# Performance work log

Hardware: AMD Instinct MI355X
Metric: run time of the kernel (lower is better)

Reference implementation:

```python
import jax, jax.numpy as jnp
import numpy as np

D_MODEL = 1024
N_EXPERTS = 8
HIDDEN = ((int(round(D_MODEL * (8.0 / 3.0))) + 63) // 64) * 64  # 2752
ALPHA = 0.05  # load_balance_alpha


def setup_inputs() -> dict:
    key = jax.random.key(0)
    ks = jax.random.split(key, 6)
    s = 0.02
    x = jax.random.normal(ks[0], (4, 1024, D_MODEL), dtype=jnp.float32)
    Wg = jax.random.normal(ks[1], (D_MODEL, N_EXPERTS), dtype=jnp.float32) * s
    bg = jnp.zeros((N_EXPERTS,), dtype=jnp.float32)
    Wu = jax.random.normal(ks[2], (N_EXPERTS, D_MODEL, HIDDEN), dtype=jnp.float32) * s
    Wv = jax.random.normal(ks[3], (N_EXPERTS, D_MODEL, HIDDEN), dtype=jnp.float32) * s
    Wd = jax.random.normal(ks[4], (N_EXPERTS, HIDDEN, D_MODEL), dtype=jnp.float32) * s
    return {"x": x, "Wg": Wg, "bg": bg, "Wu": Wu, "Wv": Wv, "Wd": Wd}


def reference(x, Wg, bg, Wu, Wv, Wd):
    b, t, d = x.shape
    E = Wu.shape[0]
    xf = x.reshape(b * t, d)  # [N, d]

    # Top-1 router
    logits = xf @ Wg + bg                      # [N, E]
    probs = jax.nn.softmax(logits, axis=-1)
    top1_idx = jnp.argmax(probs, axis=-1)      # [N]
    top1_p = jnp.max(probs, axis=-1)           # [N]
    onehot = jax.nn.one_hot(top1_idx, E, dtype=x.dtype)  # [N, E]

    # Load-balancing aux loss (both me and ce are under no_grad in the original)
    me = jax.lax.stop_gradient(onehot.mean(axis=0))
    ce = jax.lax.stop_gradient(probs.mean(axis=0))
    aux = ALPHA * E * jnp.sum(me * ce)

    # Dropless dispatch: masked per-expert SwiGLU (loop over small fixed E)
    gate = onehot * top1_p[:, None]            # [N, E] combine weights
    y = jnp.zeros_like(xf)
    for e in range(E):
        u = xf @ Wu[e]                         # [N, H]
        v = xf @ Wv[e]                         # [N, H]
        ye = (jax.nn.silu(u) * v) @ Wd[e]      # [N, d]
        y = y + gate[:, e, None] * ye

    return y.reshape(b, t, d), aux
```

## Files before the change

kernel.cpp:

```cpp
#include <hip/hip_runtime.h>

#define D_MODEL 1024
#define HID     2752
#define NEXP    8
#define NTOK    4096
#define ALPHA   0.05f

#define TILES_UV  (43 * 16 * 16)
#define TILES_WD  (16 * 43 * 8)
#define RTR_BLKS  1024

#define TS 66

typedef __bf16 bf16_t;
typedef bf16_t bf16x8 __attribute__((ext_vector_type(8)));
typedef float  f32x4  __attribute__((ext_vector_type(4)));
typedef float  vf4    __attribute__((ext_vector_type(4)));

__device__ inline unsigned short f2bf(float f) {
    unsigned int u = __float_as_uint(f);
    u += 0x7fffu + ((u >> 16) & 1u);
    return (unsigned short)(u >> 16);
}

__device__ inline bf16x8 ldsFrag(const unsigned short* p) {
    union { uint4 u; bf16x8 b; } t;
    t.u = *(const uint4*)p;
    return t.b;
}

__device__ inline void gload_lds16(const void* g, void* l) {
    __builtin_amdgcn_global_load_lds((const __attribute__((address_space(1))) void*)g,
                                     (__attribute__((address_space(3))) void*)l, 16, 0, 0);
}

__global__ __launch_bounds__(256) void prep_kernel(
    const float* __restrict__ x, const float* __restrict__ Wg, const float* __restrict__ bg,
    const float* __restrict__ Wu, const float* __restrict__ Wv, const float* __restrict__ Wd,
    unsigned short* __restrict__ WuT, unsigned short* __restrict__ WvT,
    unsigned short* __restrict__ WdT,
    int* __restrict__ eidx, float* __restrict__ gate_p,
    int* __restrict__ counts, float* __restrict__ ce_sum,
    unsigned short* __restrict__ xbf, int nTiles) {

    __shared__ __align__(16) unsigned short tile[64 * TS];
    const int id = blockIdx.x;
    const int tid = threadIdx.x;

    if (id < nTiles) {
        const int z  = id / 688;
        const int rm = id - z * 688;
        const int bx = rm % 43;
        const int by = rm / 43;
        const float* src;
        unsigned short* dst;
        int R, C, r0, c0;
        if (z < 16) {
            const int e = z & 7;
            src = ((z < 8) ? Wu : Wv) + (size_t)e * D_MODEL * HID;
            dst = ((z < 8) ? WuT : WvT) + (size_t)e * D_MODEL * HID;
            R = D_MODEL; C = HID;
            r0 = by * 64; c0 = bx * 64;
        } else {
            const int e = z - 16;
            src = Wd + (size_t)e * HID * D_MODEL;
            dst = WdT + (size_t)e * HID * D_MODEL;
            R = HID; C = D_MODEL;
            r0 = bx * 64; c0 = by * 64;
        }
#pragma unroll
        for (int j = 0; j < 4; ++j) {
            int f = j * 256 + tid;
            int row = f >> 4, c4 = (f & 15) * 4;
            vf4 v = __builtin_nontemporal_load(
                (const vf4*)(src + (size_t)(r0 + row) * C + c0 + c4));
            unsigned int p0 = (unsigned)f2bf(v.x) | ((unsigned)f2bf(v.y) << 16);
            unsigned int p1 = (unsigned)f2bf(v.z) | ((unsigned)f2bf(v.w) << 16);
            unsigned int* tp = (unsigned int*)&tile[row * TS + c4];
            tp[0] = p0; tp[1] = p1;
        }
        __syncthreads();
#pragma unroll
        for (int j = 0; j < 2; ++j) {
            int f = j * 256 + tid;
            int oc = f >> 3, kc = f & 7;
            unsigned int w[4];
#pragma unroll
            for (int q = 0; q < 4; ++q) {
                unsigned int lo = tile[(kc * 8 + 2 * q)     * TS + oc];
                unsigned int hi = tile[(kc * 8 + 2 * q + 1) * TS + oc];
                w[q] = lo | (hi << 16);
            }
            uint4 out; out.x = w[0]; out.y = w[1]; out.z = w[2]; out.w = w[3];
            *(uint4*)(dst + (size_t)(c0 + oc) * R + r0 + kc * 8) = out;
        }
        return;
    }

    float* ceS = (float*)tile;
    int*   cntS = (int*)tile + 8;
    if (tid < 8) { ceS[tid] = 0.f; cntS[tid] = 0; }
    __syncthreads();

    const int rid = id - nTiles;
    const int wid = tid >> 6, lane = tid & 63;
    const int t = rid * 4 + wid;
    const float* xr = x + (size_t)t * D_MODEL;
    unsigned short* xbr = xbf + (size_t)t * D_MODEL;

    float acc[8];
#pragma unroll
    for (int e = 0; e < 8; ++e) acc[e] = 0.f;

#pragma unroll
    for (int c = 0; c < 4; ++c) {
        int i0 = c * 256 + lane * 4;
        float4 xv = *(const float4*)(xr + i0);
        uint2 pk;
        pk.x = (unsigned)f2bf(xv.x) | ((unsigned)f2bf(xv.y) << 16);
        pk.y = (unsigned)f2bf(xv.z) | ((unsigned)f2bf(xv.w) << 16);
        *(uint2*)(xbr + i0) = pk;
#pragma unroll
        for (int j = 0; j < 4; ++j) {
            const float* wr = Wg + (size_t)(i0 + j) * 8;
            float4 lo = *(const float4*)(wr);
            float4 hi = *(const float4*)(wr + 4);
            float xs = (&xv.x)[j];
            acc[0] += xs * lo.x; acc[1] += xs * lo.y;
            acc[2] += xs * lo.z; acc[3] += xs * lo.w;
            acc[4] += xs * hi.x; acc[5] += xs * hi.y;
            acc[6] += xs * hi.z; acc[7] += xs * hi.w;
        }
    }
#pragma unroll
    for (int e = 0; e < 8; ++e) {
#pragma unroll
        for (int off = 32; off > 0; off >>= 1)
            acc[e] += __shfl_xor(acc[e], off, 64);
    }

    if (lane == 0) {
        float lg[8];
#pragma unroll
        for (int e = 0; e < 8; ++e) lg[e] = acc[e] + bg[e];
        float mx = lg[0]; int am = 0;
#pragma unroll
        for (int e = 1; e < 8; ++e) { if (lg[e] > mx) { mx = lg[e]; am = e; } }
        float ex[8], s = 0.f;
#pragma unroll
        for (int e = 0; e < 8; ++e) { ex[e] = __expf(lg[e] - mx); s += ex[e]; }
        float inv = 1.f / s;
#pragma unroll
        for (int e = 0; e < 8; ++e) atomicAdd(&ceS[e], ex[e] * inv);
        atomicAdd(&cntS[am], 1);
        eidx[t] = am;
        gate_p[t] = ex[am] * inv;
    }
    __syncthreads();
    if (tid < 8) atomicAdd(&ce_sum[tid], ceS[tid]);
    if (tid >= 8 && tid < 16) atomicAdd(&counts[tid - 8], cntS[tid - 8]);
}

__global__ __launch_bounds__(256) void transpose_kernel(const float* __restrict__ in,
                                                        unsigned short* __restrict__ out,
                                                        int R, int C) {
    __shared__ float tile[64 * 65];
    const int e = blockIdx.z;
    const float* src = in + (size_t)e * R * C;
    unsigned short* dst = out + (size_t)e * R * C;
    const int c0 = blockIdx.x * 64, r0 = blockIdx.y * 64;
    const int tid = threadIdx.x;
#pragma unroll
    for (int j = 0; j < 4; ++j) {
        int f = j * 256 + tid;
        int row = f >> 4, c4 = f & 15;
        float4 v = *(const float4*)(src + (size_t)(r0 + row) * C + c0 + c4 * 4);
        float* t = &tile[row * 65 + c4 * 4];
        t[0] = v.x; t[1] = v.y; t[2] = v.z; t[3] = v.w;
    }
    __syncthreads();
#pragma unroll
    for (int j = 0; j < 2; ++j) {
        int f = j * 256 + tid;
        int orow = f >> 3, kc = f & 7;
        unsigned short pk[8];
#pragma unroll
        for (int q = 0; q < 8; ++q) pk[q] = f2bf(tile[(kc * 8 + q) * 65 + orow]);
        *(uint4*)(dst + (size_t)(c0 + orow) * R + r0 + kc * 8) = *(uint4*)pk;
    }
}

__global__ void offsets_aux_kernel(const int* __restrict__ counts, const float* __restrict__ ce_sum,
                                   int* __restrict__ offs, float* __restrict__ aux_out) {
    if (threadIdx.x == 0) {
        int off = 0; float aux = 0.f;
        for (int e = 0; e < 8; ++e) {
            offs[e] = off; off += counts[e];
            aux += ((float)counts[e] / (float)NTOK) * (ce_sum[e] / (float)NTOK);
        }
        aux_out[0] = ALPHA * (float)NEXP * aux;
    }
}

__global__ void scatter_kernel(const int* __restrict__ eidx, const int* __restrict__ offs,
                               int* __restrict__ fill, int* __restrict__ toks) {
    int t = blockIdx.x * 256 + threadIdx.x;
    int e = eidx[t];
    int pos = atomicAdd(&fill[e], 1);
    toks[offs[e] + pos] = t;
}

__global__ __launch_bounds__(256, 2) void gemm1_kernel(
    const unsigned short* __restrict__ WuT, const unsigned short* __restrict__ WvT,
    const unsigned short* __restrict__ xbf,
    const int* __restrict__ toks, const int* __restrict__ counts, const int* __restrict__ offs,
    unsigned short* __restrict__ hbuf) {
    const int e = blockIdx.z;
    const int Ne = counts[e];
    const int mt = blockIdx.y;
    if (mt * 128 >= Ne) return;
    const int nt = blockIdx.x;
    const int slot0 = offs[e] + mt * 128;
    const int rowsV = min(128, Ne - mt * 128);
    const int ncol0 = nt * 128;
    const int colsV = min(128, HID - ncol0);

    __shared__ unsigned short As[128 * 64];
    __shared__ unsigned short Bus[128 * 64];
    __shared__ unsigned short Bvs[128 * 64];

    const int tid = threadIdx.x;

    const unsigned short* aS[4];
    const unsigned short* buS[4];
    const unsigned short* bvS[4];
    unsigned short* aD[4];
    unsigned short* buD[4];
    unsigned short* bvD[4];
#pragma unroll
    for (int i = 0; i < 4; ++i) {
        int c = i * 256 + tid;
        int r = c >> 3, ch = c & 7;
        int srcOff = ((ch ^ (r & 7)) * 8);
        int ar = min(r, rowsV - 1);
        int tok = toks[slot0 + ar];
        aS[i] = xbf + (size_t)tok * D_MODEL + srcOff;
        int bn = ncol0 + min(r, colsV - 1);
        buS[i] = WuT + ((size_t)e * HID + bn) * D_MODEL + srcOff;
        bvS[i] = WvT + ((size_t)e * HID + bn) * D_MODEL + srcOff;
        aD[i]  = As  + c * 8;
        buD[i] = Bus + c * 8;
        bvD[i] = Bvs + c * 8;
    }

    f32x4 accU[4][4], accV[4][4];
#pragma unroll
    for (int m = 0; m < 4; ++m)
#pragma unroll
        for (int n = 0; n < 4; ++n) {
            accU[m][n] = (f32x4){0.f, 0.f, 0.f, 0.f};
            accV[m][n] = (f32x4){0.f, 0.f, 0.f, 0.f};
        }

    const int lane = tid & 63;
    const int w = tid >> 6;
    const int rbase = (w >> 1) * 64;
    const int cbase = (w & 1) * 64;
    const int lrow = lane & 15;
    const int lchunk = lane >> 4;

    for (int ks = 0; ks < 16; ++ks) {
#pragma unroll
        for (int i = 0; i < 4; ++i) gload_lds16(aS[i],  aD[i]);
#pragma unroll
        for (int i = 0; i < 4; ++i) gload_lds16(buS[i], buD[i]);
#pragma unroll
        for (int i = 0; i < 4; ++i) gload_lds16(bvS[i], bvD[i]);
#pragma unroll
        for (int i = 0; i < 4; ++i) { aS[i] += 64; buS[i] += 64; bvS[i] += 64; }
        __syncthreads();

#pragma unroll
        for (int kk = 0; kk < 2; ++kk) {
            const int g = kk * 4 + lchunk;
            bf16x8 af[4], bu[4], bv[4];
#pragma unroll
            for (int m = 0; m < 4; ++m) {
                int r = rbase + m * 16 + lrow;
                af[m] = ldsFrag(&As[r * 64 + ((g ^ (r & 7)) * 8)]);
            }
#pragma unroll
            for (int n = 0; n < 4; ++n) {
                int rn = cbase + n * 16 + lrow;
                int off = rn * 64 + ((g ^ (rn & 7)) * 8);
                bu[n] = ldsFrag(&Bus[off]);
                bv[n] = ldsFrag(&Bvs[off]);
            }
#pragma unroll
            for (int m = 0; m < 4; ++m)
#pragma unroll
                for (int n = 0; n < 4; ++n) {
                    accU[m][n] = __builtin_amdgcn_mfma_f32_16x16x32_bf16(af[m], bu[n], accU[m][n], 0, 0, 0);
                    accV[m][n] = __builtin_amdgcn_mfma_f32_16x16x32_bf16(af[m], bv[n], accV[m][n], 0, 0, 0);
                }
        }
        __syncthreads();
    }

#pragma unroll
    for (int m = 0; m < 4; ++m) {
#pragma unroll
        for (int i = 0; i < 4; ++i) {
            int r = rbase + m * 16 + (lane >> 4) * 4 + i;
            if (r >= rowsV) continue;
            size_t rowOff = (size_t)(slot0 + r) * HID + ncol0;
#pragma unroll
            for (int n = 0; n < 4; ++n) {
                int c = cbase + n * 16 + (lane & 15);
                if (c < colsV) {
                    float u = accU[m][n][i];
                    float v = accV[m][n][i];
                    float s = u / (1.f + __expf(-u));
                    hbuf[rowOff + c] = f2bf(s * v);
                }
            }
        }
    }
}


#define G2_STAGE(AS, BS)                                                  \
    {                                                                     \
        _Pragma("unroll")                                                 \
        for (int i = 0; i < 4; ++i) { gload_lds16(aS[i], &AS[aOff[i]]); aS[i] += 64; } \
        _Pragma("unroll")                                                 \
        for (int i = 0; i < 2; ++i) { gload_lds16(bS[i], &BS[bOff[i]]); bS[i] += 64; } \
    }

#define G2_COMPUTE(AS, BS)                                                \
    {                                                                     \
        _Pragma("unroll")                                                 \
        for (int kk = 0; kk < 2; ++kk) {                                  \
            const int g = kk * 4 + lchunk;                                \
            bf16x8 af[4], bf[2];                                          \
            _Pragma("unroll")                                             \
            for (int m = 0; m < 4; ++m) {                                 \
                int r = rbase + m * 16 + lrow;                            \
                af[m] = ldsFrag(&AS[r * 64 + ((g ^ (r & 7)) * 8)]);       \
            }                                                             \
            _Pragma("unroll")                                             \
            for (int n = 0; n < 2; ++n) {                                 \
                int rn = cbase + n * 16 + lrow;                           \
                bf[n] = ldsFrag(&BS[rn * 64 + ((g ^ (rn & 7)) * 8)]);     \
            }                                                             \
            __builtin_amdgcn_s_setprio(1);                                \
            _Pragma("unroll")                                             \
            for (int m = 0; m < 4; ++m)                                   \
                _Pragma("unroll")                                         \
                for (int n = 0; n < 2; ++n)                               \
                    acc[m][n] = __builtin_amdgcn_mfma_f32_16x16x32_bf16(af[m], bf[n], acc[m][n], 0, 0, 0); \
            __builtin_amdgcn_s_setprio(0);                                \
        }                                                                 \
    }

__global__ __launch_bounds__(256, 2) void gemm2_kernel(
    const unsigned short* __restrict__ WdT, const unsigned short* __restrict__ hbuf,
    const int* __restrict__ toks, const int* __restrict__ counts, const int* __restrict__ offs,
    const float* __restrict__ gate_p, float* __restrict__ yout) {
    const int id = blockIdx.x;
    const int e  = id & 7;
    const int j  = id >> 3;
    const int mt = j & 31;
    const int nt = j >> 5;
    const int Ne = counts[e];
    if (mt * 128 >= Ne) return;
    const int slot0 = offs[e] + mt * 128;
    const int rowsV = min(128, Ne - mt * 128);
    const int ncol0 = nt * 64;

    __shared__ unsigned short As0[128 * 64];
    __shared__ unsigned short As1[128 * 64];
    __shared__ unsigned short Bs0[64 * 64];
    __shared__ unsigned short Bs1[64 * 64];

    const int tid = threadIdx.x;

    const unsigned short* aS[4];
    int aOff[4];
#pragma unroll
    for (int i = 0; i < 4; ++i) {
        int c = i * 256 + tid;
        int r = c >> 3, ch = c & 7;
        int srcOff = (ch ^ (r & 7)) * 8;
        int ar = min(r, rowsV - 1);
        aS[i] = hbuf + (size_t)(slot0 + ar) * HID + srcOff;
        aOff[i] = c * 8;
    }
    const unsigned short* bS[2];
    int bOff[2];
#pragma unroll
    for (int i = 0; i < 2; ++i) {
        int c = i * 256 + tid;
        int r = c >> 3, ch = c & 7;
        int srcOff = (ch ^ (r & 7)) * 8;
        bS[i] = WdT + ((size_t)e * D_MODEL + ncol0 + r) * HID + srcOff;
        bOff[i] = c * 8;
    }

    f32x4 acc[4][2];
#pragma unroll
    for (int m = 0; m < 4; ++m)
#pragma unroll
        for (int n = 0; n < 2; ++n) acc[m][n] = (f32x4){0.f, 0.f, 0.f, 0.f};

    const int lane = tid & 63;
    const int w = tid >> 6;
    const int rbase = (w >> 1) * 64;
    const int cbase = (w & 1) * 32;
    const int lrow = lane & 15;
    const int lchunk = lane >> 4;

    G2_STAGE(As0, Bs0);
    __syncthreads();

#pragma unroll 1
    for (int k2 = 0; k2 < 21; ++k2) {
        G2_STAGE(As1, Bs1);
        G2_COMPUTE(As0, Bs0);
        __syncthreads();
        G2_STAGE(As0, Bs0);
        G2_COMPUTE(As1, Bs1);
        __syncthreads();
    }
    G2_COMPUTE(As0, Bs0);

#pragma unroll
    for (int m = 0; m < 4; ++m) {
#pragma unroll
        for (int i = 0; i < 4; ++i) {
            int r = rbase + m * 16 + (lane >> 4) * 4 + i;
            if (r >= rowsV) continue;
            int tok = toks[slot0 + r];
            float p = gate_p[tok];
            float* yrow = yout + (size_t)tok * D_MODEL + ncol0;
#pragma unroll
            for (int n = 0; n < 2; ++n) {
                int c = cbase + n * 16 + (lane & 15);
                yrow[c] = p * acc[m][n][i];
            }
        }
    }
}

extern "C" void kernel_launch(void* const* d_in, const int* in_sizes, int n_in,
                              void* d_out, int out_size, void* d_ws, size_t ws_size,
                              hipStream_t stream) {
    const float* x  = (const float*)d_in[0];
    const float* Wg = (const float*)d_in[1];
    const float* bg = (const float*)d_in[2];
    const float* Wu = (const float*)d_in[3];
    const float* Wv = (const float*)d_in[4];
    const float* Wd = (const float*)d_in[5];
    float* yout = (float*)d_out;
    float* aux_out = yout + (size_t)NTOK * D_MODEL;

    char* ws = (char*)d_ws;
    int*   counts = (int*)(ws + 0);
    int*   offs   = (int*)(ws + 32);
    float* ce_sum = (float*)(ws + 64);
    int*   fill   = (int*)(ws + 96);
    int*   eidx   = (int*)(ws + 128);
    float* gate_p = (float*)(ws + 16512);
    int*   toks   = (int*)(ws + 32896);
    unsigned short* xbf  = (unsigned short*)(ws + 65536);
    unsigned short* hbuf = (unsigned short*)(ws + 8454144);
    unsigned short* WuT  = (unsigned short*)(ws + 30998528);
    unsigned short* WvT  = (unsigned short*)(ws + 76087296);
    const size_t WDT_OFF = 121176064;
    const size_t WDT_SZ  = (size_t)NEXP * D_MODEL * HID * 2;
    const bool sepWdT = ws_size >= WDT_OFF + WDT_SZ;
    unsigned short* WdT = sepWdT ? (unsigned short*)(ws + WDT_OFF) : WuT;

    const int nTiles = sepWdT ? (TILES_UV + TILES_WD) : TILES_UV;

    (void)hipMemsetAsync(ws, 0, 128, stream);
    prep_kernel<<<nTiles + RTR_BLKS, 256, 0, stream>>>(
        x, Wg, bg, Wu, Wv, Wd, WuT, WvT, WdT,
        eidx, gate_p, counts, ce_sum, xbf, nTiles);
    offsets_aux_kernel<<<1, 64, 0, stream>>>(counts, ce_sum, offs, aux_out);
    scatter_kernel<<<16, 256, 0, stream>>>(eidx, offs, fill, toks);
    gemm1_kernel<<<dim3(22, 32, 8), 256, 0, stream>>>(WuT, WvT, xbf, toks, counts, offs, hbuf);
    if (!sepWdT)
        transpose_kernel<<<dim3(D_MODEL / 64, HID / 64, 8), 256, 0, stream>>>(Wd, WdT, HID, D_MODEL);
    gemm2_kernel<<<8 * 32 * 16, 256, 0, stream>>>(WdT, hbuf, toks, counts, offs, gate_p, yout);
}
```

Before: 252.0 us.

## Double-buffer gemm1 with 128x64 tiles, fine-grained waitcnt sync, fuse offsets into scatter

Gemm1 switches from 128x128 single-buffered tiles to 128x64 tiles with double-buffered LDS. Global-to-LDS loads for the next k-step now overlap MFMA compute, using explicit vmcnt waits, raw barriers and sched barriers. MFMA issue runs at raised priority. Gemm2 swaps __syncthreads for the same partial vmcnt waits. The offsets/aux kernel is folded into the scatter kernel, which removes one launch. The smaller N tile doubles A (x) reloads and the grid size, and the hand-written waitcnt counts are fragile if the number of loads changes.

```diff
diff --git a/kernel.cpp b/kernel.cpp
--- a/kernel.cpp
+++ b/kernel.cpp
@@ -16,6 +16,13 @@
 typedef bf16_t bf16x8 __attribute__((ext_vector_type(8)));
 typedef float  f32x4  __attribute__((ext_vector_type(4)));
 typedef float  vf4    __attribute__((ext_vector_type(4)));
+
+#define VM_WAIT8  asm volatile("s_waitcnt vmcnt(8)" ::: "memory")
+#define VM_WAIT6  asm volatile("s_waitcnt vmcnt(6)" ::: "memory")
+#define VM_WAIT0  asm volatile("s_waitcnt vmcnt(0)" ::: "memory")
+#define LGKM0     asm volatile("s_waitcnt lgkmcnt(0)" ::: "memory")
+#define SBAR      __builtin_amdgcn_s_barrier()
+#define SCHED0    __builtin_amdgcn_sched_barrier(0)
 
 __device__ inline unsigned short f2bf(float f) {
     unsigned int u = __float_as_uint(f);
@@ -190,74 +197,125 @@
     }
 }
 
-__global__ void offsets_aux_kernel(const int* __restrict__ counts, const float* __restrict__ ce_sum,
-                                   int* __restrict__ offs, float* __restrict__ aux_out) {
-    if (threadIdx.x == 0) {
+__global__ void scatter_kernel(const int* __restrict__ eidx, const int* __restrict__ counts,
+                               const float* __restrict__ ce_sum,
+                               int* __restrict__ offs, float* __restrict__ aux_out,
+                               int* __restrict__ fill, int* __restrict__ toks) {
+    __shared__ int offS[8];
+    const int tid = threadIdx.x;
+    if (tid == 0) {
         int off = 0; float aux = 0.f;
+#pragma unroll
         for (int e = 0; e < 8; ++e) {
-            offs[e] = off; off += counts[e];
+            offS[e] = off;
+            if (blockIdx.x == 0) offs[e] = off;
+            off += counts[e];
             aux += ((float)counts[e] / (float)NTOK) * (ce_sum[e] / (float)NTOK);
         }
-        aux_out[0] = ALPHA * (float)NEXP * aux;
-    }
-}
-
-__global__ void scatter_kernel(const int* __restrict__ eidx, const int* __restrict__ offs,
-                               int* __restrict__ fill, int* __restrict__ toks) {
-    int t = blockIdx.x * 256 + threadIdx.x;
+        if (blockIdx.x == 0) aux_out[0] = ALPHA * (float)NEXP * aux;
+    }
+    __syncthreads();
+    int t = blockIdx.x * 256 + tid;
     int e = eidx[t];
     int pos = atomicAdd(&fill[e], 1);
-    toks[offs[e] + pos] = t;
-}
+    toks[offS[e] + pos] = t;
+}
+
+
+#define G1_STAGE(AS, BUS, BVS)                                            \
+    {                                                                     \
+        _Pragma("unroll")                                                 \
+        for (int i = 0; i < 4; ++i) { gload_lds16(aS[i], &AS[aOff[i]]); aS[i] += 64; } \
+        _Pragma("unroll")                                                 \
+        for (int i = 0; i < 2; ++i) {                                     \
+            gload_lds16(buS[i], &BUS[bOff[i]]); buS[i] += 64;             \
+            gload_lds16(bvS[i], &BVS[bOff[i]]); bvS[i] += 64;             \
+        }                                                                 \
+    }
+
+#define G1_COMPUTE(AS, BUS, BVS)                                          \
+    {                                                                     \
+        _Pragma("unroll")                                                 \
+        for (int kk = 0; kk < 2; ++kk) {                                  \
+            const int g = kk * 4 + lchunk;                                \
+            bf16x8 af[4], bu[2], bv[2];                                   \
+            _Pragma("unroll")                                             \
+            for (int m = 0; m < 4; ++m) {                                 \
+                int r = rbase + m * 16 + lrow;                            \
+                af[m] = ldsFrag(&AS[r * 64 + ((g ^ (r & 7)) * 8)]);       \
+            }                                                             \
+            _Pragma("unroll")                                             \
+            for (int n = 0; n < 2; ++n) {                                 \
+                int rn = cbase + n * 16 + lrow;                           \
+                int off = rn * 64 + ((g ^ (rn & 7)) * 8);                 \
+                bu[n] = ldsFrag(&BUS[off]);                               \
+                bv[n] = ldsFrag(&BVS[off]);                               \
+            }                                                             \
+            __builtin_amdgcn_s_setprio(1);                                \
+            _Pragma("unroll")                                             \
+            for (int m = 0; m < 4; ++m)                                   \
+                _Pragma("unroll")                                         \
+                for (int n = 0; n < 2; ++n) {                             \
+                    accU[m][n] = __builtin_amdgcn_mfma_f32_16x16x32_bf16(af[m], bu[n], accU[m][n], 0, 0, 0); \
+                    accV[m][n] = __builtin_amdgcn_mfma_f32_16x16x32_bf16(af[m], bv[n], accV[m][n], 0, 0, 0); \
+                }                                                         \
+            __builtin_amdgcn_s_setprio(0);                                \
+        }                                                                 \
+    }
 
 __global__ __launch_bounds__(256, 2) void gemm1_kernel(
     const unsigned short* __restrict__ WuT, const unsigned short* __restrict__ WvT,
     const unsigned short* __restrict__ xbf,
     const int* __restrict__ toks, const int* __restrict__ counts, const int* __restrict__ offs,
     unsigned short* __restrict__ hbuf) {
-    const int e = blockIdx.z;
+    const int e  = blockIdx.z;
+    const int mt = blockIdx.y;
+    const int nt = blockIdx.x;
     const int Ne = counts[e];
-    const int mt = blockIdx.y;
     if (mt * 128 >= Ne) return;
-    const int nt = blockIdx.x;
     const int slot0 = offs[e] + mt * 128;
     const int rowsV = min(128, Ne - mt * 128);
-    const int ncol0 = nt * 128;
-    const int colsV = min(128, HID - ncol0);
-
-    __shared__ unsigned short As[128 * 64];
-    __shared__ unsigned short Bus[128 * 64];
-    __shared__ unsigned short Bvs[128 * 64];
+    const int ncol0 = nt * 64;
+
+    __shared__ unsigned short As0[128 * 64];
+    __shared__ unsigned short As1[128 * 64];
+    __shared__ unsigned short Bus0[64 * 64];
+    __shared__ unsigned short Bus1[64 * 64];
+    __shared__ unsigned short Bvs0[64 * 64];
+    __shared__ unsigned short Bvs1[64 * 64];
 
     const int tid = threadIdx.x;
 
     const unsigned short* aS[4];
-    const unsigned short* buS[4];
-    const unsigned short* bvS[4];
-    unsigned short* aD[4];
-    unsigned short* buD[4];
-    unsigned short* bvD[4];
+    int aOff[4];
 #pragma unroll
     for (int i = 0; i < 4; ++i) {
         int c = i * 256 + tid;
         int r = c >> 3, ch = c & 7;
-        int srcOff = ((ch ^ (r & 7)) * 8);
+        int srcOff = (ch ^ (r & 7)) * 8;
         int ar = min(r, rowsV - 1);
         int tok = toks[slot0 + ar];
         aS[i] = xbf + (size_t)tok * D_MODEL + srcOff;
-        int bn = ncol0 + min(r, colsV - 1);
+        aOff[i] = c * 8;
+    }
+    const unsigned short *buS[2], *bvS[2];
+    int bOff[2];
+#pragma unroll
+    for (int i = 0; i < 2; ++i) {
+        int c = i * 256 + tid;
+        int r = c >> 3, ch = c & 7;
+        int srcOff = (ch ^ (r & 7)) * 8;
+        int bn = ncol0 + r;
         buS[i] = WuT + ((size_t)e * HID + bn) * D_MODEL + srcOff;
         bvS[i] = WvT + ((size_t)e * HID + bn) * D_MODEL + srcOff;
-        aD[i]  = As  + c * 8;
-        buD[i] = Bus + c * 8;
-        bvD[i] = Bvs + c * 8;
-    }
-
-    f32x4 accU[4][4], accV[4][4];
+        bOff[i] = c * 8;
+    }
+
+    f32x4 accU[4][2], accV[4][2];
 #pragma unroll
     for (int m = 0; m < 4; ++m)
 #pragma unroll
-        for (int n = 0; n < 4; ++n) {
+        for (int n = 0; n < 2; ++n) {
             accU[m][n] = (f32x4){0.f, 0.f, 0.f, 0.f};
             accV[m][n] = (f32x4){0.f, 0.f, 0.f, 0.f};
         }
@@ -265,47 +323,29 @@
     const int lane = tid & 63;
     const int w = tid >> 6;
     const int rbase = (w >> 1) * 64;
-    const int cbase = (w & 1) * 64;
+    const int cbase = (w & 1) * 32;
     const int lrow = lane & 15;
     const int lchunk = lane >> 4;
 
-    for (int ks = 0; ks < 16; ++ks) {
-#pragma unroll
-        for (int i = 0; i < 4; ++i) gload_lds16(aS[i],  aD[i]);
-#pragma unroll
-        for (int i = 0; i < 4; ++i) gload_lds16(buS[i], buD[i]);
-#pragma unroll
-        for (int i = 0; i < 4; ++i) gload_lds16(bvS[i], bvD[i]);
-#pragma unroll
-        for (int i = 0; i < 4; ++i) { aS[i] += 64; buS[i] += 64; bvS[i] += 64; }
-        __syncthreads();
-
-#pragma unroll
-        for (int kk = 0; kk < 2; ++kk) {
-            const int g = kk * 4 + lchunk;
-            bf16x8 af[4], bu[4], bv[4];
-#pragma unroll
-            for (int m = 0; m < 4; ++m) {
-                int r = rbase + m * 16 + lrow;
-                af[m] = ldsFrag(&As[r * 64 + ((g ^ (r & 7)) * 8)]);
-            }
-#pragma unroll
-            for (int n = 0; n < 4; ++n) {
-                int rn = cbase + n * 16 + lrow;
-                int off = rn * 64 + ((g ^ (rn & 7)) * 8);
-                bu[n] = ldsFrag(&Bus[off]);
-                bv[n] = ldsFrag(&Bvs[off]);
-            }
-#pragma unroll
-            for (int m = 0; m < 4; ++m)
-#pragma unroll
-                for (int n = 0; n < 4; ++n) {
-                    accU[m][n] = __builtin_amdgcn_mfma_f32_16x16x32_bf16(af[m], bu[n], accU[m][n], 0, 0, 0);
-                    accV[m][n] = __builtin_amdgcn_mfma_f32_16x16x32_bf16(af[m], bv[n], accV[m][n], 0, 0, 0);
-                }
-        }
-        __syncthreads();
-    }
+    G1_STAGE(As0, Bus0, Bvs0);
+
+#pragma unroll 1
+    for (int k2 = 0; k2 < 7; ++k2) {
+        G1_STAGE(As1, Bus1, Bvs1);
+        VM_WAIT8; SBAR; SCHED0;
+        G1_COMPUTE(As0, Bus0, Bvs0);
+        SCHED0; LGKM0; SBAR;
+        G1_STAGE(As0, Bus0, Bvs0);
+        VM_WAIT8; SBAR; SCHED0;
+        G1_COMPUTE(As1, Bus1, Bvs1);
+        SCHED0; LGKM0; SBAR;
+    }
+    G1_STAGE(As1, Bus1, Bvs1);
+    VM_WAIT8; SBAR; SCHED0;
+    G1_COMPUTE(As0, Bus0, Bvs0);
+    SCHED0; LGKM0; SBAR;
+    VM_WAIT0; SBAR; SCHED0;
+    G1_COMPUTE(As1, Bus1, Bvs1);
 
 #pragma unroll
     for (int m = 0; m < 4; ++m) {
@@ -315,14 +355,12 @@
             if (r >= rowsV) continue;
             size_t rowOff = (size_t)(slot0 + r) * HID + ncol0;
 #pragma unroll
-            for (int n = 0; n < 4; ++n) {
+            for (int n = 0; n < 2; ++n) {
                 int c = cbase + n * 16 + (lane & 15);
-                if (c < colsV) {
-                    float u = accU[m][n][i];
-                    float v = accV[m][n][i];
-                    float s = u / (1.f + __expf(-u));
-                    hbuf[rowOff + c] = f2bf(s * v);
-                }
+                float u = accU[m][n][i];
+                float v = accV[m][n][i];
+                float s = u / (1.f + __expf(-u));
+                hbuf[rowOff + c] = f2bf(s * v);
             }
         }
     }
@@ -421,17 +459,19 @@
     const int lchunk = lane >> 4;
 
     G2_STAGE(As0, Bs0);
-    __syncthreads();
 
 #pragma unroll 1
     for (int k2 = 0; k2 < 21; ++k2) {
         G2_STAGE(As1, Bs1);
+        VM_WAIT6; SBAR; SCHED0;
         G2_COMPUTE(As0, Bs0);
-        __syncthreads();
+        SCHED0; LGKM0; SBAR;
         G2_STAGE(As0, Bs0);
+        VM_WAIT6; SBAR; SCHED0;
         G2_COMPUTE(As1, Bs1);
-        __syncthreads();
-    }
+        SCHED0; LGKM0; SBAR;
+    }
+    VM_WAIT0; SBAR; SCHED0;
     G2_COMPUTE(As0, Bs0);
 
 #pragma unroll
@@ -487,9 +527,8 @@
     prep_kernel<<<nTiles + RTR_BLKS, 256, 0, stream>>>(
         x, Wg, bg, Wu, Wv, Wd, WuT, WvT, WdT,
         eidx, gate_p, counts, ce_sum, xbf, nTiles);
-    offsets_aux_kernel<<<1, 64, 0, stream>>>(counts, ce_sum, offs, aux_out);
-    scatter_kernel<<<16, 256, 0, stream>>>(eidx, offs, fill, toks);
-    gemm1_kernel<<<dim3(22, 32, 8), 256, 0, stream>>>(WuT, WvT, xbf, toks, counts, offs, hbuf);
+    scatter_kernel<<<16, 256, 0, stream>>>(eidx, counts, ce_sum, offs, aux_out, fill, toks);
+    gemm1_kernel<<<dim3(43, 32, 8), 256, 0, stream>>>(WuT, WvT, xbf, toks, counts, offs, hbuf);
     if (!sepWdT)
         transpose_kernel<<<dim3(D_MODEL / 64, HID / 64, 8), 256, 0, stream>>>(Wd, WdT, HID, D_MODEL);
     gemm2_kernel<<<8 * 32 * 16, 256, 0, stream>>>(WdT, hbuf, toks, counts, offs, gate_p, yout);
```

Result: no change. 251.1 us (-0.3%).
